# Performance work log

Hardware: AMD Instinct MI355X
Metric: run time of the kernel (lower is better)

## Reference

```python
import jax, jax.numpy as jnp
import numpy as np

C_ATOM = 128; C_PAIR = 16; H = 4; DH = 32; BQ = 32; BK = 128
N_ATOMS = 11776; NB = N_ATOMS // BQ; N_TOK = 512
C_TOK = 384; C_TP = 128; C_TP_IN = 32; N_LAYERS = 3

def _ln(x):
    mu = jnp.mean(x, axis=-1, keepdims=True)
    xc = x - mu
    var = jnp.mean(xc * xc, axis=-1, keepdims=True)
    return xc * jax.lax.rsqrt(var + 1e-5)

def setup_inputs():
    key = jax.random.key(0)
    ks = jax.random.split(key, 32)
    rn = lambda k, s, sc=0.02: jax.random.normal(k, s, jnp.float32) * sc
    q_idx = jnp.arange(N_ATOMS, dtype=jnp.int32).reshape(NB, BQ)
    centers = jnp.arange(NB, dtype=jnp.int32) * BQ + BQ // 2
    win = centers[:, None] + jnp.arange(-BK // 2, BK // 2, dtype=jnp.int32)[None, :]
    k_mask = (win >= 0) & (win < N_ATOMS)
    k_idx = jnp.clip(win, 0, N_ATOMS - 1)
    return {
        'atom_feats': jax.random.normal(ks[0], (1, N_ATOMS, C_ATOM), jnp.float32),
        'token_pair_feats': jax.random.normal(ks[1], (1, N_TOK, N_TOK, C_TP_IN), jnp.float32),
        'W_cond': rn(ks[2], (C_ATOM, C_ATOM)),
        'W_ph': rn(ks[3], (C_PAIR, C_ATOM)),
        'W_pw': rn(ks[4], (C_PAIR, C_ATOM)),
        'W_mlp1': rn(ks[5], (C_PAIR, C_PAIR)),
        'W_mlp2': rn(ks[6], (C_PAIR, C_PAIR)),
        'pb_ln_w': jnp.ones((C_PAIR,), jnp.float32),
        'pb_ln_b': jnp.zeros((C_PAIR,), jnp.float32),
        'pb_w': rn(ks[7], (H, C_PAIR)),
        'sln_w': rn(ks[8], (N_LAYERS, 2 * C_ATOM, C_ATOM)),
        'qkv_w': rn(ks[9], (N_LAYERS, 3 * C_ATOM, C_ATOM)),
        'q_bias': rn(ks[10], (N_LAYERS, C_ATOM)),
        'out_w': rn(ks[11], (N_LAYERS, C_ATOM, C_ATOM)),
        'out_b': jnp.zeros((N_LAYERS, C_ATOM), jnp.float32),
        'ada_w': rn(ks[12], (N_LAYERS, 2 * C_ATOM, C_ATOM)),
        'ta_w': rn(ks[13], (N_LAYERS, 4 * C_ATOM, C_ATOM)),
        'tb_w': rn(ks[14], (N_LAYERS, C_ATOM, 2 * C_ATOM)),
        'gate_w': rn(ks[15], (N_LAYERS, C_ATOM, C_ATOM)),
        'gate_b': jnp.full((N_LAYERS, C_ATOM), -2.0, jnp.float32),
        'W_tok': rn(ks[16], (C_TOK, C_ATOM)),
        'W_trunk': rn(ks[17], (C_TOK, C_TOK)),
        'W_struct': rn(ks[18], (C_TOK, C_TOK)),
        'W_pairin': rn(ks[19], (C_TP, C_TP_IN)),
        'W_outer': rn(ks[20], (2 * C_TP, C_TOK)),
        'q_idx': q_idx, 'k_idx': k_idx, 'k_mask': k_mask,
        'atom_to_token': jnp.sort(jax.random.randint(ks[21], (N_ATOMS,), 0, N_TOK, dtype=jnp.int32)),
    }

def _forward(atom_feats, token_pair_feats, W_cond, W_ph, W_pw, W_mlp1, W_mlp2,
             pb_ln_w, pb_ln_b, pb_w, sln_w, qkv_w, q_bias, out_w, out_b,
             ada_w, ta_w, tb_w, gate_w, gate_b, W_tok, W_trunk, W_struct,
             W_pairin, W_outer, q_idx, k_idx, k_mask, atom_to_token):
    c = atom_feats @ W_cond.T                       # [1,N,128] atom conditioning
    s_ln = _ln(c)                                   # shared normed conditioning
    # ---- blocked pair representation + pair-to-bias ----
    cq = jax.nn.relu(s_ln[:, q_idx])                # [1,NB,BQ,128]
    ck = jax.nn.relu(s_ln[:, k_idx])                # [1,NB,BK,128]
    p = (cq @ W_ph.T)[:, :, :, None, :] + (ck @ W_pw.T)[:, :, None, :, :]  # [1,NB,BQ,BK,16]
    p = p + jax.nn.relu(jax.nn.relu(p) @ W_mlp1.T) @ W_mlp2.T
    pb = (_ln(p) * pb_ln_w + pb_ln_b) @ pb_w.T      # [1,NB,BQ,BK,H]
    pb = jnp.transpose(pb, (0, 1, 4, 2, 3))         # [1,NB,H,BQ,BK]
    neg = jnp.where(k_mask[None, :, None, None, :], 0.0, -1e9)
    a = c
    scale = 1.0 / np.sqrt(DH).astype(np.float32)
    for l in range(N_LAYERS):
        # blocked local attention with AdaLN-conditioned input
        gb = s_ln @ sln_w[l].T
        x = jax.nn.sigmoid(gb[..., :C_ATOM]) * _ln(a) + gb[..., C_ATOM:]
        qkv = x @ qkv_w[l].T
        q, k, v = jnp.split(qkv, 3, axis=-1)
        q = (q + q_bias[l]).reshape(1, N_ATOMS, H, DH)
        k = k.reshape(1, N_ATOMS, H, DH)
        v = v.reshape(1, N_ATOMS, H, DH)
        qb = q[:, q_idx]; kb = k[:, k_idx]; vb = v[:, k_idx]
        sc = jnp.einsum('bnqhd,bnkhd->bnhqk', qb, kb) * scale + pb + neg
        att = jax.nn.softmax(sc, axis=-1)
        o = jnp.einsum('bnhqk,bnkhd->bnqhd', att, vb).reshape(1, N_ATOMS, C_ATOM)
        a = a + o @ out_w[l].T + out_b[l]
        # AdaLN-modulated SwiGLU transition with adaLN-zero gate (bias init -2)
        gb2 = s_ln @ ada_w[l].T
        xt = jax.nn.sigmoid(gb2[..., :C_ATOM]) * _ln(a) + gb2[..., C_ATOM:]
        ab = xt @ ta_w[l].T
        g = jax.nn.silu(ab[..., :2 * C_ATOM]) * ab[..., 2 * C_ATOM:]
        h = g @ tb_w[l].T
        gate = jax.nn.sigmoid(s_ln @ gate_w[l].T + gate_b[l])
        a = a + gate * h
    # ---- atom -> token aggregation and output projections ----
    atom_out = jax.nn.relu(a @ W_tok.T)             # [1,N,384]
    sums = jax.ops.segment_sum(atom_out[0], atom_to_token, num_segments=N_TOK)
    cnt = jax.ops.segment_sum(jnp.ones((N_ATOMS,), atom_out.dtype), atom_to_token, num_segments=N_TOK)
    tok = (sums / jnp.maximum(cnt, 1.0)[:, None])[None]  # [1,T,384]
    s_trunk = tok @ W_trunk.T
    s_struct = tok @ W_struct.T
    u = tok @ W_outer.T                              # [1,T,256]
    pair = token_pair_feats @ W_pairin.T + u[..., :C_TP][:, :, None, :] + u[..., C_TP:][:, None, :, :]
    return s_trunk, s_struct, pair

def reference(atom_feats, token_pair_feats, W_cond, W_ph, W_pw, W_mlp1, W_mlp2,
              pb_ln_w, pb_ln_b, pb_w, sln_w, qkv_w, q_bias, out_w, out_b,
              ada_w, ta_w, tb_w, gate_w, gate_b, W_tok, W_trunk, W_struct,
              W_pairin, W_outer, q_idx, k_idx, k_mask, atom_to_token):
    return _forward(atom_feats, token_pair_feats, W_cond, W_ph, W_pw, W_mlp1, W_mlp2,
                    pb_ln_w, pb_ln_b, pb_w, sln_w, qkv_w, q_bias, out_w, out_b,
                    ada_w, ta_w, tb_w, gate_w, gate_b, W_tok, W_trunk, W_struct,
                    W_pairin, W_outer, q_idx, k_idx, k_mask, atom_to_token)
```

## Files before the change

### kernel.cpp

```cpp
#include <hip/hip_runtime.h>
#include <cstddef>

typedef unsigned short u16;
typedef __attribute__((ext_vector_type(8))) short bf8;
typedef __attribute__((ext_vector_type(4))) float f4;
typedef __attribute__((ext_vector_type(4))) unsigned short us4;

#define NATOMS 11776
#define NBLK   368

__device__ __forceinline__ u16 f2b(float x){
  union { float f; unsigned u; } v; v.f = x;
  unsigned r = v.u + 0x7fffu + ((v.u >> 16) & 1u);
  return (u16)(r >> 16);
}
__device__ __forceinline__ float b2f(u16 x){
  union { unsigned u; float f; } v; v.u = ((unsigned)x) << 16;
  return v.f;
}
__device__ __forceinline__ f4 f4zero(){ f4 z = {0.f,0.f,0.f,0.f}; return z; }
__device__ __forceinline__ f4 mfma16(bf8 a, bf8 b, f4 c){
  return __builtin_amdgcn_mfma_f32_16x16x32_bf16(a, b, c, 0, 0, 0);
}
__device__ __forceinline__ int iclamp(int v, int lo, int hi){ return v < lo ? lo : (v > hi ? hi : v); }
__device__ __forceinline__ void lds_fence(){
  asm volatile("s_waitcnt lgkmcnt(0)" ::: "memory");
  __builtin_amdgcn_sched_barrier(0);
}
__device__ __forceinline__ bf8 cvt_f32x8(const float* __restrict__ p){
  float4 a = *(const float4*)p, b = *(const float4*)(p + 4);
  bf8 o;
  o[0] = (short)f2b(a.x); o[1] = (short)f2b(a.y); o[2] = (short)f2b(a.z); o[3] = (short)f2b(a.w);
  o[4] = (short)f2b(b.x); o[5] = (short)f2b(b.y); o[6] = (short)f2b(b.z); o[7] = (short)f2b(b.w);
  return o;
}

struct CvtArgs {
  const float* src[11];
  u16* dst[11];
  int n4[11];
};

__global__ __launch_bounds__(256) void k_convert(CvtArgs a){
  int stride = gridDim.x * 256;
  int tid = blockIdx.x * 256 + threadIdx.x;
  for (int s = 0; s < 11; ++s){
    const float4* src = (const float4*)a.src[s];
    us4* dst = (us4*)a.dst[s];
    int n = a.n4[s];
    for (int i = tid; i < n; i += stride){
      float4 v = src[i];
      us4 o;
      o.x = f2b(v.x); o.y = f2b(v.y); o.z = f2b(v.z); o.w = f2b(v.w);
      dst[i] = o;
    }
  }
}

template<int N, int K, int LDA = K>
__device__ __forceinline__ void gemm_strip(const u16* __restrict__ A, const u16* __restrict__ W, float* L){
  constexpr int CPW = N / 4;
  constexpr int T = CPW / 16;
  const int lane = threadIdx.x & 63;
  const int wave = threadIdx.x >> 6;
  const int rr = lane & 15, grp = lane >> 4;
  f4 acc[T];
#pragma unroll
  for (int t = 0; t < T; ++t) acc[t] = f4zero();
#pragma unroll
  for (int kc = 0; kc < K / 32; ++kc){
    bf8 af = *(const bf8*)(A + rr * LDA + kc * 32 + grp * 8);
#pragma unroll
    for (int t = 0; t < T; ++t){
      const u16* wp = W + (size_t)(wave * CPW + t * 16 + rr) * K + kc * 32 + grp * 8;
      acc[t] = mfma16(af, *(const bf8*)wp, acc[t]);
    }
  }
#pragma unroll
  for (int t = 0; t < T; ++t)
#pragma unroll
    for (int r = 0; r < 4; ++r)
      L[(grp * 4 + r) * N + wave * CPW + t * 16 + rr] = acc[t][r];
}

__global__ __launch_bounds__(256) void k_cond(const float* __restrict__ af, const float* __restrict__ Wc,
                                              const float* __restrict__ Wph, const float* __restrict__ Wpw,
                                              float* __restrict__ a_f, float* __restrict__ lnA,
                                              u16* __restrict__ sln_bf, float* __restrict__ ph,
                                              float* __restrict__ pw){
  __shared__ float LB[16 * 128];
  __shared__ __align__(16) u16 X[16 * 136];
  const int strip = blockIdx.x;
  const int lane = threadIdx.x & 63, wave = threadIdx.x >> 6;
  const int rr = lane & 15, grp = lane >> 4;
  {
    f4 acc[2];
    acc[0] = f4zero(); acc[1] = f4zero();
#pragma unroll
    for (int kc = 0; kc < 4; ++kc){
      bf8 afr = cvt_f32x8(af + (size_t)(strip * 16 + rr) * 128 + kc * 32 + grp * 8);
#pragma unroll
      for (int t = 0; t < 2; ++t){
        bf8 bfr = cvt_f32x8(Wc + (size_t)(wave * 32 + t * 16 + rr) * 128 + kc * 32 + grp * 8);
        acc[t] = mfma16(afr, bfr, acc[t]);
      }
    }
#pragma unroll
    for (int t = 0; t < 2; ++t)
#pragma unroll
      for (int r = 0; r < 4; ++r)
        LB[(grp * 4 + r) * 128 + wave * 32 + t * 16 + rr] = acc[t][r];
  }
  __syncthreads();
  {
    int r = threadIdx.x >> 4, s = threadIdx.x & 15;
    float sum = 0.f, sq = 0.f;
#pragma unroll
    for (int j = 0; j < 8; ++j){ float v = LB[r * 128 + s * 8 + j]; sum += v; sq += v * v; }
#pragma unroll
    for (int m = 1; m < 16; m <<= 1){ sum += __shfl_xor(sum, m); sq += __shfl_xor(sq, m); }
    float mu = sum * (1.f / 128.f);
    float var = sq * (1.f / 128.f) - mu * mu;
    float rs = rsqrtf(var + 1e-5f);
#pragma unroll
    for (int j = 0; j < 8; ++j){
      int c = s * 8 + j;
      float v = LB[r * 128 + c];
      size_t idx = (size_t)(strip * 16 + r) * 128 + c;
      a_f[idx] = v;
      float ln = (v - mu) * rs;
      lnA[idx] = ln;
      sln_bf[idx] = f2b(ln);
      X[r * 136 + c] = f2b(fmaxf(ln, 0.f));
    }
  }
  __syncthreads();
  if (wave < 2){
    const float* Wsel = wave ? Wpw : Wph;
    f4 acc = f4zero();
#pragma unroll
    for (int kc = 0; kc < 4; ++kc){
      bf8 afr = *(const bf8*)(&X[rr * 136 + kc * 32 + grp * 8]);
      bf8 bfr = cvt_f32x8(Wsel + (size_t)rr * 128 + kc * 32 + grp * 8);
      acc = mfma16(afr, bfr, acc);
    }
    float* out = wave ? pw : ph;
#pragma unroll
    for (int r = 0; r < 4; ++r)
      out[(size_t)(strip * 16 + grp * 4 + r) * 16 + rr] = acc[r];
  }
}

__global__ __launch_bounds__(256) void k_pre(const u16* __restrict__ sln, const float* __restrict__ lnA,
                                             const u16* __restrict__ slnW, const u16* __restrict__ qkvW,
                                             const float* __restrict__ qb, u16* __restrict__ qkv_out){
  __shared__ float LB[16 * 384];
  __shared__ __align__(16) u16 X[16 * 136];
  const int strip = blockIdx.x;
  const u16* Ag = sln + (size_t)strip * 2048;
  gemm_strip<256, 128>(Ag, slnW, LB);
  __syncthreads();
  for (int i = threadIdx.x; i < 2048; i += 256){
    int r = i >> 7, c = i & 127;
    float g1 = LB[r * 256 + c], g2 = LB[r * 256 + 128 + c];
    float s = 1.f / (1.f + __expf(-g1));
    X[r * 136 + c] = f2b(s * lnA[(size_t)(strip * 16 + r) * 128 + c] + g2);
  }
  __syncthreads();
  gemm_strip<384, 128, 136>(X, qkvW, LB);
  __syncthreads();
  const float scale = 0.17677669529663687f;
  for (int i = threadIdx.x; i < 16 * 384; i += 256){
    int r = i / 384, c = i - r * 384;
    float v = LB[i];
    if (c < 128) v = (v + qb[c]) * scale;
    qkv_out[(size_t)(strip * 16 + r) * 384 + c] = f2b(v);
  }
}

template<int LAST>
__global__ __launch_bounds__(256) void k_post(const u16* __restrict__ sln, float* __restrict__ lnA,
                                              float* __restrict__ a,
                                              const u16* __restrict__ gateW, const float* __restrict__ gbias,
                                              const u16* __restrict__ adaW, const u16* __restrict__ taW,
                                              const u16* __restrict__ tbW, const u16* __restrict__ tokW,
                                              float* __restrict__ atom_out){
  __shared__ float LB[16 * 512];
  __shared__ __align__(16) u16 X[16 * 136];
  __shared__ __align__(16) u16 G[16 * 264];
  const int strip = blockIdx.x;
  const u16* Ag = sln + (size_t)strip * 2048;
  float gv[8];
  gemm_strip<128, 128>(Ag, gateW, LB);
  __syncthreads();
#pragma unroll
  for (int ii = 0; ii < 8; ++ii){
    int i = threadIdx.x + 256 * ii;
    int c = i & 127;
    gv[ii] = 1.f / (1.f + __expf(-(LB[i] + gbias[c])));
  }
  __syncthreads();
  gemm_strip<256, 128>(Ag, adaW, LB);
  __syncthreads();
  for (int i = threadIdx.x; i < 2048; i += 256){
    int r = i >> 7, c = i & 127;
    float g1 = LB[r * 256 + c], g2 = LB[r * 256 + 128 + c];
    float s = 1.f / (1.f + __expf(-g1));
    X[r * 136 + c] = f2b(s * lnA[(size_t)(strip * 16 + r) * 128 + c] + g2);
  }
  __syncthreads();
  gemm_strip<512, 128, 136>(X, taW, LB);
  __syncthreads();
  for (int i = threadIdx.x; i < 16 * 256; i += 256){
    int r = i >> 8, c = i & 255;
    float ab1 = LB[r * 512 + c], ab2 = LB[r * 512 + 256 + c];
    G[r * 264 + c] = f2b(ab1 / (1.f + __expf(-ab1)) * ab2);
  }
  __syncthreads();
  gemm_strip<128, 256, 264>(G, tbW, LB);
  __syncthreads();
#pragma unroll
  for (int ii = 0; ii < 8; ++ii){
    int i = threadIdx.x + 256 * ii;
    size_t idx = (size_t)strip * 2048 + i;
    float v = a[idx] + gv[ii] * LB[i];
    a[idx] = v;
    LB[i] = v;
    if (LAST){ int r = i >> 7, c = i & 127; X[r * 136 + c] = f2b(v); }
  }
  __syncthreads();
  if (!LAST){
    int r = threadIdx.x >> 4, s = threadIdx.x & 15;
    float sum = 0.f, sq = 0.f;
#pragma unroll
    for (int j = 0; j < 8; ++j){ float v = LB[r * 128 + s * 8 + j]; sum += v; sq += v * v; }
#pragma unroll
    for (int m = 1; m < 16; m <<= 1){ sum += __shfl_xor(sum, m); sq += __shfl_xor(sq, m); }
    float mu = sum * (1.f / 128.f);
    float var = sq * (1.f / 128.f) - mu * mu;
    float rs = rsqrtf(var + 1e-5f);
#pragma unroll
    for (int j = 0; j < 8; ++j){
      int c = s * 8 + j;
      lnA[(size_t)(strip * 16 + r) * 128 + c] = (LB[r * 128 + c] - mu) * rs;
    }
  } else {
    gemm_strip<384, 128, 136>(X, tokW, LB);
    __syncthreads();
    const size_t base = (size_t)strip * 16 * 384;
    for (int i = threadIdx.x; i < 16 * 384; i += 256) atom_out[base + i] = fmaxf(LB[i], 0.f);
  }
}

__global__ __launch_bounds__(256) void k_pb(const float* __restrict__ ph, const float* __restrict__ pw,
                                            const float* __restrict__ W1, const float* __restrict__ W2,
                                            const float* __restrict__ lnw, const float* __restrict__ lnb,
                                            const float* __restrict__ pbw, float* __restrict__ bias){
  __shared__ __align__(16) u16 mt[4][16 * 24];
  __shared__ __align__(16) u16 vt[4][16 * 24];
  const int t = threadIdx.x;
  const int lane = t & 63, wave = t >> 6;
  const int rr = lane & 15, grp = lane >> 4;
  const int b = blockIdx.x >> 3, qg = blockIdx.x & 7;
  const int q = qg * 4 + wave;
  const int qa = b * 32 + q;

  bf8 wf1 = {0,0,0,0,0,0,0,0}, wf2 = {0,0,0,0,0,0,0,0};
  bf8 bproj = {0,0,0,0,0,0,0,0}, bones = {0,0,0,0,0,0,0,0};
  if (grp < 2){
#pragma unroll
    for (int j = 0; j < 8; ++j){
      wf1[j] = (short)f2b(W1[rr * 16 + grp * 8 + j]);
      wf2[j] = (short)f2b(W2[rr * 16 + grp * 8 + j]);
      bones[j] = (short)0x3F80;
    }
    if (rr < 4){
#pragma unroll
      for (int j = 0; j < 8; ++j)
        bproj[j] = (short)f2b(pbw[rr * 16 + grp * 8 + j] * lnw[grp * 8 + j]);
    }
  }
  float w2s_r = 0.f, bb_r = 0.f;
  if (rr < 4){
#pragma unroll
    for (int cc = 0; cc < 16; ++cc){
      float pv = pbw[rr * 16 + cc];
      w2s_r += pv * lnw[cc];
      bb_r  += pv * lnb[cc];
    }
  }
  const float* phq = ph + (size_t)qa * 16;
  float pha[8];
  if (grp < 2){
#pragma unroll
    for (int j = 0; j < 8; ++j) pha[j] = phq[grp * 8 + j];
  }
  const float ph_r = phq[rr];
  u16* mw = &mt[wave][0];
  u16* vw = &vt[wave][0];

  for (int kt = 0; kt < 8; ++kt){
    const int k0 = kt * 16;
    bf8 af = {0,0,0,0,0,0,0,0};
    if (grp < 2){
      int winA = b * 32 + k0 + rr - 48;
      int kaA = iclamp(winA, 0, NATOMS - 1);
      const float* pwr = pw + (size_t)kaA * 16 + grp * 8;
#pragma unroll
      for (int j = 0; j < 8; ++j) af[j] = (short)f2b(fmaxf(pha[j] + pwr[j], 0.f));
    }
    f4 c1 = mfma16(af, wf1, f4zero());
#pragma unroll
    for (int r = 0; r < 4; ++r)
      mw[(grp * 4 + r) * 24 + rr] = f2b(fmaxf(c1[r], 0.f));
    lds_fence();
    bf8 mf = {0,0,0,0,0,0,0,0};
    if (grp < 2) mf = *(const bf8*)(mw + rr * 24 + grp * 8);
    f4 c2 = mfma16(mf, wf2, f4zero());
#pragma unroll
    for (int r = 0; r < 4; ++r){
      int win = b * 32 + k0 + grp * 4 + r - 48;
      int ka = iclamp(win, 0, NATOMS - 1);
      float v = c2[r] + ph_r + pw[(size_t)ka * 16 + rr];
      vw[(grp * 4 + r) * 24 + rr] = f2b(v);
    }
    lds_fence();
    bf8 vf = {0,0,0,0,0,0,0,0}, vf2 = {0,0,0,0,0,0,0,0};
    if (grp < 2){
      vf = *(const bf8*)(vw + rr * 24 + grp * 8);
#pragma unroll
      for (int j = 0; j < 8; ++j){
        float x = b2f((u16)vf[j]);
        union { float f; unsigned u; } s; s.f = x * x;
        vf2[j] = (short)(u16)(s.u >> 16);
      }
    }
    f4 T1 = mfma16(vf, bproj, f4zero());
    f4 T2 = mfma16(vf, bones, f4zero());
    f4 T3 = mfma16(vf2, bones, f4zero());
    if (rr < 4){
      float4 o;
      float ov[4];
#pragma unroll
      for (int r = 0; r < 4; ++r){
        int win = b * 32 + k0 + grp * 4 + r - 48;
        bool valid = (win >= 0) && (win < NATOMS);
        float S = T2[r], Q = T3[r], d = T1[r];
        float mu = S * (1.f / 16.f);
        float var = Q * (1.f / 16.f) - mu * mu;
        float rq = rsqrtf(var + 1e-5f);
        ov[r] = rq * (d - mu * w2s_r) + bb_r + (valid ? 0.f : -1e9f);
      }
      o.x = ov[0]; o.y = ov[1]; o.z = ov[2]; o.w = ov[3];
      *(float4*)(bias + ((size_t)((b * 4 + rr) * 32) + q) * 128 + k0 + grp * 4) = o;
    }
  }
}

__global__ __launch_bounds__(256) void k_attn(const u16* __restrict__ qkv, const float* __restrict__ bias,
                                              const u16* __restrict__ outw, const float* __restrict__ outb,
                                              float* __restrict__ a, float* __restrict__ lnA){
  __shared__ u16 VT[128][136];
  __shared__ u16 P[4][32 * 136];
  __shared__ u16 O[32][136];
  __shared__ float part2[32][8];
  const int t = threadIdx.x;
  const int lane = t & 63, wave = t >> 6;
  const int b = blockIdx.x;
  const int rr = lane & 15, grp = lane >> 4;

  for (int i = 0; i < 8; ++i){
    int s = t + 256 * i;
    int ka = s & 127, d0 = (s >> 7) * 8;
    int win = b * 32 + ka - 48;
    int src = iclamp(win, 0, NATOMS - 1);
    bf8 v = *(const bf8*)(qkv + (size_t)src * 384 + 256 + d0);
#pragma unroll
    for (int j = 0; j < 8; ++j) VT[d0 + j][ka] = (u16)v[j];
  }
  __syncthreads();

  const int h = wave;
  bf8 kfr[8];
#pragma unroll
  for (int kt = 0; kt < 8; ++kt){
    int ka = kt * 16 + rr;
    int win = b * 32 + ka - 48;
    int src = iclamp(win, 0, NATOMS - 1);
    kfr[kt] = *(const bf8*)(qkv + (size_t)src * 384 + 128 + h * 32 + grp * 8);
  }
  f4 S[2][8];
#pragma unroll
  for (int qt = 0; qt < 2; ++qt){
    bf8 qf = *(const bf8*)(qkv + (size_t)(b * 32 + qt * 16 + rr) * 384 + h * 32 + grp * 8);
#pragma unroll
    for (int kt = 0; kt < 8; ++kt){
      S[qt][kt] = f4zero();
      S[qt][kt] = mfma16(qf, kfr[kt], S[qt][kt]);
    }
  }
  const float* brow = bias + (size_t)((b * 4 + h) * 32) * 128;
#pragma unroll
  for (int qt = 0; qt < 2; ++qt){
#pragma unroll
    for (int r = 0; r < 4; ++r){
      int q = qt * 16 + grp * 4 + r;
      float vals[8];
      float mx = -1e30f;
#pragma unroll
      for (int kt = 0; kt < 8; ++kt){
        float v = S[qt][kt][r] + brow[q * 128 + kt * 16 + rr];
        vals[kt] = v;
        mx = fmaxf(mx, v);
      }
#pragma unroll
      for (int m = 1; m < 16; m <<= 1) mx = fmaxf(mx, __shfl_xor(mx, m));
      float sum = 0.f;
#pragma unroll
      for (int kt = 0; kt < 8; ++kt){ vals[kt] = __expf(vals[kt] - mx); sum += vals[kt]; }
#pragma unroll
      for (int m = 1; m < 16; m <<= 1) sum += __shfl_xor(sum, m);
      float inv = 1.f / sum;
#pragma unroll
      for (int kt = 0; kt < 8; ++kt)
        P[h][q * 136 + kt * 16 + rr] = f2b(vals[kt] * inv);
    }
  }
  __syncthreads();
  f4 oacc[2][2];
#pragma unroll
  for (int qt = 0; qt < 2; ++qt)
#pragma unroll
    for (int dt = 0; dt < 2; ++dt) oacc[qt][dt] = f4zero();
#pragma unroll
  for (int kc = 0; kc < 4; ++kc){
#pragma unroll
    for (int qt = 0; qt < 2; ++qt){
      bf8 pa = *(const bf8*)(&P[h][(qt * 16 + rr) * 136 + kc * 32 + grp * 8]);
#pragma unroll
      for (int dt = 0; dt < 2; ++dt){
        bf8 vb = *(const bf8*)(&VT[h * 32 + dt * 16 + rr][kc * 32 + grp * 8]);
        oacc[qt][dt] = mfma16(pa, vb, oacc[qt][dt]);
      }
    }
  }
#pragma unroll
  for (int qt = 0; qt < 2; ++qt)
#pragma unroll
    for (int dt = 0; dt < 2; ++dt)
#pragma unroll
      for (int r = 0; r < 4; ++r)
        O[qt * 16 + grp * 4 + r][h * 32 + dt * 16 + rr] = f2b(oacc[qt][dt][r]);
  __syncthreads();
  f4 pacc[2][2];
#pragma unroll
  for (int qt = 0; qt < 2; ++qt)
#pragma unroll
    for (int ct = 0; ct < 2; ++ct) pacc[qt][ct] = f4zero();
#pragma unroll
  for (int kc = 0; kc < 4; ++kc){
    bf8 a0 = *(const bf8*)(&O[rr][kc * 32 + grp * 8]);
    bf8 a1 = *(const bf8*)(&O[16 + rr][kc * 32 + grp * 8]);
#pragma unroll
    for (int ct = 0; ct < 2; ++ct){
      bf8 wf = *(const bf8*)(outw + (size_t)(wave * 32 + ct * 16 + rr) * 128 + kc * 32 + grp * 8);
      pacc[0][ct] = mfma16(a0, wf, pacc[0][ct]);
      pacc[1][ct] = mfma16(a1, wf, pacc[1][ct]);
    }
  }
  float vv[2][2][4];
#pragma unroll
  for (int qt = 0; qt < 2; ++qt)
#pragma unroll
    for (int ct = 0; ct < 2; ++ct)
#pragma unroll
      for (int r = 0; r < 4; ++r){
        int q = qt * 16 + grp * 4 + r;
        int col = wave * 32 + ct * 16 + rr;
        size_t idx = (size_t)(b * 32 + q) * 128 + col;
        float v = a[idx] + pacc[qt][ct][r] + outb[col];
        a[idx] = v;
        vv[qt][ct][r] = v;
      }
#pragma unroll
  for (int qt = 0; qt < 2; ++qt)
#pragma unroll
    for (int r = 0; r < 4; ++r){
      float ps = vv[qt][0][r] + vv[qt][1][r];
      float pq = vv[qt][0][r] * vv[qt][0][r] + vv[qt][1][r] * vv[qt][1][r];
#pragma unroll
      for (int m = 1; m < 16; m <<= 1){ ps += __shfl_xor(ps, m); pq += __shfl_xor(pq, m); }
      if (rr == 0){
        int q = qt * 16 + grp * 4 + r;
        part2[q][wave * 2] = ps;
        part2[q][wave * 2 + 1] = pq;
      }
    }
  __syncthreads();
#pragma unroll
  for (int qt = 0; qt < 2; ++qt)
#pragma unroll
    for (int r = 0; r < 4; ++r){
      int q = qt * 16 + grp * 4 + r;
      f4 p0 = *(const f4*)&part2[q][0];
      f4 p1 = *(const f4*)&part2[q][4];
      float S = p0[0] + p0[2] + p1[0] + p1[2];
      float Q = p0[1] + p0[3] + p1[1] + p1[3];
      float mu = S * (1.f / 128.f);
      float var = Q * (1.f / 128.f) - mu * mu;
      float rs = rsqrtf(var + 1e-5f);
#pragma unroll
      for (int ct = 0; ct < 2; ++ct){
        int col = wave * 32 + ct * 16 + rr;
        lnA[(size_t)(b * 32 + q) * 128 + col] = (vv[qt][ct][r] - mu) * rs;
      }
    }
}

__device__ __forceinline__ int lbound(const int* __restrict__ arr, int n, int v){
  int lo = 0, hi = n;
  while (lo < hi){ int mid = (lo + hi) >> 1; if (arr[mid] < v) lo = mid + 1; else hi = mid; }
  return lo;
}

__global__ __launch_bounds__(256) void k_segmean(const float* __restrict__ atom_out,
                                                 const int* __restrict__ a2t, u16* __restrict__ tokbf){
  const int tok = blockIdx.x;
  __shared__ int lo_s, hi_s;
  if (threadIdx.x == 0){
    lo_s = lbound(a2t, NATOMS, tok);
    hi_s = lbound(a2t, NATOMS, tok + 1);
  }
  __syncthreads();
  int lo = lo_s, hi = hi_s;
  float inv = 1.f / fmaxf((float)(hi - lo), 1.f);
  for (int c = threadIdx.x; c < 384; c += 256){
    float s = 0.f;
    for (int aa = lo; aa < hi; ++aa) s += atom_out[(size_t)aa * 384 + c];
    tokbf[(size_t)tok * 384 + c] = f2b(s * inv);
  }
}

__global__ __launch_bounds__(256) void k_tok(const u16* __restrict__ tok, const u16* __restrict__ catW,
                                             float* __restrict__ s_trunk, float* __restrict__ s_struct,
                                             float* __restrict__ u_f){
  __shared__ float LB[16 * 1024];
  const int strip = blockIdx.x;
  gemm_strip<1024, 384>(tok + (size_t)strip * 16 * 384, catW, LB);
  __syncthreads();
  for (int i = threadIdx.x; i < 16 * 1024; i += 256){
    int r = i >> 10, c = i & 1023;
    int row = strip * 16 + r;
    float v = LB[i];
    if (c < 384) s_trunk[(size_t)row * 384 + c] = v;
    else if (c < 768) s_struct[(size_t)row * 384 + (c - 384)] = v;
    else u_f[(size_t)row * 256 + (c - 768)] = v;
  }
}

__global__ __launch_bounds__(256) void k_pair(const float* __restrict__ tpf, const float* __restrict__ Wp,
                                              const float* __restrict__ u, float* __restrict__ out){
  const int lane = threadIdx.x & 63, wave = threadIdx.x >> 6;
  const int rr = lane & 15, grp = lane >> 4;
  const int pairbase = blockIdx.x * 64 + wave * 16;
  const int i = (blockIdx.x * 64) >> 9;
  bf8 af;
  {
    const float* tr = tpf + (size_t)(pairbase + rr) * 32 + grp * 8;
#pragma unroll
    for (int j = 0; j < 8; ++j) af[j] = (short)f2b(tr[j]);
  }
  f4 acc[8];
#pragma unroll
  for (int t = 0; t < 8; ++t){
    bf8 bf;
    const float* wr = Wp + (size_t)(t * 16 + rr) * 32 + grp * 8;
#pragma unroll
    for (int j = 0; j < 8; ++j) bf[j] = (short)f2b(wr[j]);
    acc[t] = mfma16(af, bf, f4zero());
  }
  const float* ui = u + (size_t)i * 256;
#pragma unroll
  for (int t = 0; t < 8; ++t){
    int c = t * 16 + rr;
    float uic = ui[c];
#pragma unroll
    for (int r = 0; r < 4; ++r){
      int p = pairbase + grp * 4 + r;
      int j = p & 511;
      out[(size_t)p * 128 + c] = acc[t][r] + uic + u[(size_t)j * 256 + 128 + c];
    }
  }
}

extern "C" void kernel_launch(void* const* d_in, const int* in_sizes, int n_in,
                              void* d_out, int out_size, void* d_ws, size_t ws_size,
                              hipStream_t stream){
  (void)in_sizes; (void)n_in; (void)out_size; (void)ws_size;
  const float* atom_feats = (const float*)d_in[0];
  const float* tpf        = (const float*)d_in[1];
  const float* W_cond     = (const float*)d_in[2];
  const float* W_ph       = (const float*)d_in[3];
  const float* W_pw       = (const float*)d_in[4];
  const float* W_mlp1     = (const float*)d_in[5];
  const float* W_mlp2     = (const float*)d_in[6];
  const float* pb_ln_w    = (const float*)d_in[7];
  const float* pb_ln_b    = (const float*)d_in[8];
  const float* pb_w       = (const float*)d_in[9];
  const float* sln_w      = (const float*)d_in[10];
  const float* qkv_w      = (const float*)d_in[11];
  const float* q_bias     = (const float*)d_in[12];
  const float* out_w      = (const float*)d_in[13];
  const float* out_b      = (const float*)d_in[14];
  const float* ada_w      = (const float*)d_in[15];
  const float* ta_w       = (const float*)d_in[16];
  const float* tb_w       = (const float*)d_in[17];
  const float* gate_w     = (const float*)d_in[18];
  const float* gate_b     = (const float*)d_in[19];
  const float* W_tok      = (const float*)d_in[20];
  const float* W_trunk    = (const float*)d_in[21];
  const float* W_struct   = (const float*)d_in[22];
  const float* W_pairin   = (const float*)d_in[23];
  const float* W_outer    = (const float*)d_in[24];
  const int*   a2t        = (const int*)d_in[28];

  char* wsb = (char*)d_ws;
  size_t off = 0;
  auto alc = [&](size_t bytes) -> void* {
    void* r = wsb + off;
    off = (off + bytes + 255) & ~(size_t)255;
    return r;
  };

  u16* sln_bfw   = (u16*)alc(98304 * 2);
  u16* qkv_bfw   = (u16*)alc(147456 * 2);
  u16* out_bfw   = (u16*)alc(49152 * 2);
  u16* ada_bfw   = (u16*)alc(98304 * 2);
  u16* ta_bfw    = (u16*)alc(196608 * 2);
  u16* tb_bfw    = (u16*)alc(98304 * 2);
  u16* gate_bfw  = (u16*)alc(49152 * 2);
  u16* tok_bfw   = (u16*)alc(49152 * 2);
  u16* trunk_bfw = (u16*)alc(147456 * 2);
  u16* struct_bfw= (u16*)alc(147456 * 2);
  u16* outer_bfw = (u16*)alc(98304 * 2);
  float* a_f     = (float*)alc((size_t)NATOMS * 128 * 4);
  float* lnA     = (float*)alc((size_t)NATOMS * 128 * 4);
  u16* sln_bf    = (u16*)alc((size_t)NATOMS * 128 * 2);
  u16* qkv_bf    = (u16*)alc((size_t)NATOMS * 384 * 2);
  float* ph      = (float*)alc((size_t)NATOMS * 16 * 4);
  float* pw      = (float*)alc((size_t)NATOMS * 16 * 4);
  float* bias    = (float*)alc((size_t)NBLK * 4 * 32 * 128 * 4);
  float* atom_out= bias;
  u16* tok_bf    = (u16*)alc(512 * 384 * 2);
  float* u_f     = (float*)alc(512 * 256 * 4);

  float* s_trunk  = (float*)d_out;
  float* s_struct = s_trunk + 512 * 384;
  float* pair_out = s_struct + 512 * 384;

  CvtArgs ca;
  const float* srcs[11] = {sln_w, qkv_w, out_w, ada_w, ta_w, tb_w, gate_w,
                           W_tok, W_trunk, W_struct, W_outer};
  u16* dsts[11] = {sln_bfw, qkv_bfw, out_bfw, ada_bfw, ta_bfw, tb_bfw, gate_bfw,
                   tok_bfw, trunk_bfw, struct_bfw, outer_bfw};
  int n4s[11] = {24576, 36864, 12288, 24576, 49152, 24576, 12288,
                 12288, 36864, 36864, 24576};
  for (int s = 0; s < 11; ++s){ ca.src[s] = srcs[s]; ca.dst[s] = dsts[s]; ca.n4[s] = n4s[s]; }
  k_convert<<<256, 256, 0, stream>>>(ca);

  k_cond<<<736, 256, 0, stream>>>(atom_feats, W_cond, W_ph, W_pw, a_f, lnA, sln_bf, ph, pw);
  k_pb<<<NBLK * 8, 256, 0, stream>>>(ph, pw, W_mlp1, W_mlp2, pb_ln_w, pb_ln_b, pb_w, bias);

  for (int l = 0; l < 3; ++l){
    const u16* slnW  = sln_bfw  + (size_t)l * 256 * 128;
    const u16* qkvW  = qkv_bfw  + (size_t)l * 384 * 128;
    const u16* outW  = out_bfw  + (size_t)l * 128 * 128;
    const u16* adaW  = ada_bfw  + (size_t)l * 256 * 128;
    const u16* taW   = ta_bfw   + (size_t)l * 512 * 128;
    const u16* tbW   = tb_bfw   + (size_t)l * 128 * 256;
    const u16* gateW = gate_bfw + (size_t)l * 128 * 128;
    k_pre<<<736, 256, 0, stream>>>(sln_bf, lnA, slnW, qkvW, q_bias + l * 128, qkv_bf);
    k_attn<<<NBLK, 256, 0, stream>>>(qkv_bf, bias, outW, out_b + l * 128, a_f, lnA);
    if (l < 2)
      k_post<0><<<736, 256, 0, stream>>>(sln_bf, lnA, a_f, gateW, gate_b + l * 128,
                                         adaW, taW, tbW, tok_bfw, atom_out);
    else
      k_post<1><<<736, 256, 0, stream>>>(sln_bf, lnA, a_f, gateW, gate_b + l * 128,
                                         adaW, taW, tbW, tok_bfw, atom_out);
  }

  k_segmean<<<512, 256, 0, stream>>>(atom_out, a2t, tok_bf);
  k_tok<<<32, 256, 0, stream>>>(tok_bf, trunk_bfw, s_trunk, s_struct, u_f);
  k_pair<<<4096, 256, 0, stream>>>(tpf, W_pairin, u_f, pair_out);
}
```

Before: 390.6 us.

## Fuse per-layer pre-attention projection into cond and post kernels; split token GEMM

The pre-attention kernel (adaptive LN gating plus QKV projection) is folded into the tail of the conditioning kernel for layer 0 and into the post-attention kernel for later layers. The normalized activations stay in shared memory instead of being written to lnA and read back, and three kernel launches are removed. Separately, the token projection kernel is split across four column quadrants, giving 128 blocks instead of 32 for more parallelism. The fused kernels use more shared memory per block, which may lower occupancy.

```diff
diff --git a/kernel.cpp b/kernel.cpp
--- a/kernel.cpp
+++ b/kernel.cpp
@@ -83,13 +83,17 @@
       L[(grp * 4 + r) * N + wave * CPW + t * 16 + rr] = acc[t][r];
 }
 
-__global__ __launch_bounds__(256) void k_cond(const float* __restrict__ af, const float* __restrict__ Wc,
-                                              const float* __restrict__ Wph, const float* __restrict__ Wpw,
-                                              float* __restrict__ a_f, float* __restrict__ lnA,
-                                              u16* __restrict__ sln_bf, float* __restrict__ ph,
-                                              float* __restrict__ pw){
-  __shared__ float LB[16 * 128];
-  __shared__ __align__(16) u16 X[16 * 136];
+__global__ __launch_bounds__(256) void k_cond_pre(const float* __restrict__ af, const float* __restrict__ Wc,
+                                                  const float* __restrict__ Wph, const float* __restrict__ Wpw,
+                                                  float* __restrict__ a_f, u16* __restrict__ sln_bf,
+                                                  float* __restrict__ ph, float* __restrict__ pw,
+                                                  const u16* __restrict__ slnW, const u16* __restrict__ qkvW,
+                                                  const float* __restrict__ qb, u16* __restrict__ qkv_out){
+  __shared__ float LB[16 * 384];
+  __shared__ __align__(16) u16 Xs[16 * 136];
+  __shared__ __align__(16) u16 Xr[16 * 136];
+  __shared__ __align__(16) u16 Xx[16 * 136];
+  __shared__ float LNf[16 * 128];
   const int strip = blockIdx.x;
   const int lane = threadIdx.x & 63, wave = threadIdx.x >> 6;
   const int rr = lane & 15, grp = lane >> 4;
@@ -129,45 +133,24 @@
       size_t idx = (size_t)(strip * 16 + r) * 128 + c;
       a_f[idx] = v;
       float ln = (v - mu) * rs;
-      lnA[idx] = ln;
-      sln_bf[idx] = f2b(ln);
-      X[r * 136 + c] = f2b(fmaxf(ln, 0.f));
-    }
-  }
-  __syncthreads();
-  if (wave < 2){
-    const float* Wsel = wave ? Wpw : Wph;
-    f4 acc = f4zero();
-#pragma unroll
-    for (int kc = 0; kc < 4; ++kc){
-      bf8 afr = *(const bf8*)(&X[rr * 136 + kc * 32 + grp * 8]);
-      bf8 bfr = cvt_f32x8(Wsel + (size_t)rr * 128 + kc * 32 + grp * 8);
-      acc = mfma16(afr, bfr, acc);
-    }
-    float* out = wave ? pw : ph;
-#pragma unroll
-    for (int r = 0; r < 4; ++r)
-      out[(size_t)(strip * 16 + grp * 4 + r) * 16 + rr] = acc[r];
-  }
-}
-
-__global__ __launch_bounds__(256) void k_pre(const u16* __restrict__ sln, const float* __restrict__ lnA,
-                                             const u16* __restrict__ slnW, const u16* __restrict__ qkvW,
-                                             const float* __restrict__ qb, u16* __restrict__ qkv_out){
-  __shared__ float LB[16 * 384];
-  __shared__ __align__(16) u16 X[16 * 136];
-  const int strip = blockIdx.x;
-  const u16* Ag = sln + (size_t)strip * 2048;
-  gemm_strip<256, 128>(Ag, slnW, LB);
+      LNf[r * 128 + c] = ln;
+      u16 lb = f2b(ln);
+      sln_bf[idx] = lb;
+      Xs[r * 136 + c] = lb;
+      Xr[r * 136 + c] = f2b(fmaxf(ln, 0.f));
+    }
+  }
+  __syncthreads();
+  gemm_strip<256, 128, 136>(Xs, slnW, LB);
   __syncthreads();
   for (int i = threadIdx.x; i < 2048; i += 256){
     int r = i >> 7, c = i & 127;
     float g1 = LB[r * 256 + c], g2 = LB[r * 256 + 128 + c];
     float s = 1.f / (1.f + __expf(-g1));
-    X[r * 136 + c] = f2b(s * lnA[(size_t)(strip * 16 + r) * 128 + c] + g2);
-  }
-  __syncthreads();
-  gemm_strip<384, 128, 136>(X, qkvW, LB);
+    Xx[r * 136 + c] = f2b(s * LNf[r * 128 + c] + g2);
+  }
+  __syncthreads();
+  gemm_strip<384, 128, 136>(Xx, qkvW, LB);
   __syncthreads();
   const float scale = 0.17677669529663687f;
   for (int i = threadIdx.x; i < 16 * 384; i += 256){
@@ -176,18 +159,35 @@
     if (c < 128) v = (v + qb[c]) * scale;
     qkv_out[(size_t)(strip * 16 + r) * 384 + c] = f2b(v);
   }
+  if (wave < 2){
+    const float* Wsel = wave ? Wpw : Wph;
+    f4 acc = f4zero();
+#pragma unroll
+    for (int kc = 0; kc < 4; ++kc){
+      bf8 afr = *(const bf8*)(&Xr[rr * 136 + kc * 32 + grp * 8]);
+      bf8 bfr = cvt_f32x8(Wsel + (size_t)rr * 128 + kc * 32 + grp * 8);
+      acc = mfma16(afr, bfr, acc);
+    }
+    float* out = wave ? pw : ph;
+#pragma unroll
+    for (int r = 0; r < 4; ++r)
+      out[(size_t)(strip * 16 + grp * 4 + r) * 16 + rr] = acc[r];
+  }
 }
 
 template<int LAST>
-__global__ __launch_bounds__(256) void k_post(const u16* __restrict__ sln, float* __restrict__ lnA,
-                                              float* __restrict__ a,
-                                              const u16* __restrict__ gateW, const float* __restrict__ gbias,
-                                              const u16* __restrict__ adaW, const u16* __restrict__ taW,
-                                              const u16* __restrict__ tbW, const u16* __restrict__ tokW,
-                                              float* __restrict__ atom_out){
+__global__ __launch_bounds__(256) void k_postpre(const u16* __restrict__ sln, const float* __restrict__ lnA,
+                                                 float* __restrict__ a,
+                                                 const u16* __restrict__ gateW, const float* __restrict__ gbias,
+                                                 const u16* __restrict__ adaW, const u16* __restrict__ taW,
+                                                 const u16* __restrict__ tbW,
+                                                 const u16* __restrict__ slnW2, const u16* __restrict__ qkvW2,
+                                                 const float* __restrict__ qb2, u16* __restrict__ qkv_out,
+                                                 const u16* __restrict__ tokW, float* __restrict__ atom_out){
   __shared__ float LB[16 * 512];
   __shared__ __align__(16) u16 X[16 * 136];
   __shared__ __align__(16) u16 G[16 * 264];
+  __shared__ float LNf[16 * 128];
   const int strip = blockIdx.x;
   const u16* Ag = sln + (size_t)strip * 2048;
   float gv[8];
@@ -230,19 +230,40 @@
   }
   __syncthreads();
   if (!LAST){
-    int r = threadIdx.x >> 4, s = threadIdx.x & 15;
-    float sum = 0.f, sq = 0.f;
-#pragma unroll
-    for (int j = 0; j < 8; ++j){ float v = LB[r * 128 + s * 8 + j]; sum += v; sq += v * v; }
-#pragma unroll
-    for (int m = 1; m < 16; m <<= 1){ sum += __shfl_xor(sum, m); sq += __shfl_xor(sq, m); }
-    float mu = sum * (1.f / 128.f);
-    float var = sq * (1.f / 128.f) - mu * mu;
-    float rs = rsqrtf(var + 1e-5f);
-#pragma unroll
-    for (int j = 0; j < 8; ++j){
-      int c = s * 8 + j;
-      lnA[(size_t)(strip * 16 + r) * 128 + c] = (LB[r * 128 + c] - mu) * rs;
+    {
+      int r = threadIdx.x >> 4, s = threadIdx.x & 15;
+      float sum = 0.f, sq = 0.f;
+#pragma unroll
+      for (int j = 0; j < 8; ++j){ float v = LB[r * 128 + s * 8 + j]; sum += v; sq += v * v; }
+#pragma unroll
+      for (int m = 1; m < 16; m <<= 1){ sum += __shfl_xor(sum, m); sq += __shfl_xor(sq, m); }
+      float mu = sum * (1.f / 128.f);
+      float var = sq * (1.f / 128.f) - mu * mu;
+      float rs = rsqrtf(var + 1e-5f);
+#pragma unroll
+      for (int j = 0; j < 8; ++j){
+        int c = s * 8 + j;
+        LNf[r * 128 + c] = (LB[r * 128 + c] - mu) * rs;
+      }
+    }
+    __syncthreads();
+    gemm_strip<256, 128>(Ag, slnW2, LB);
+    __syncthreads();
+    for (int i = threadIdx.x; i < 2048; i += 256){
+      int r = i >> 7, c = i & 127;
+      float g1 = LB[r * 256 + c], g2 = LB[r * 256 + 128 + c];
+      float s = 1.f / (1.f + __expf(-g1));
+      X[r * 136 + c] = f2b(s * LNf[r * 128 + c] + g2);
+    }
+    __syncthreads();
+    gemm_strip<384, 128, 136>(X, qkvW2, LB);
+    __syncthreads();
+    const float scale = 0.17677669529663687f;
+    for (int i = threadIdx.x; i < 16 * 384; i += 256){
+      int r = i / 384, c = i - r * 384;
+      float v = LB[i];
+      if (c < 128) v = (v + qb2[c]) * scale;
+      qkv_out[(size_t)(strip * 16 + r) * 384 + c] = f2b(v);
     }
   } else {
     gemm_strip<384, 128, 136>(X, tokW, LB);
@@ -544,17 +565,18 @@
 __global__ __launch_bounds__(256) void k_tok(const u16* __restrict__ tok, const u16* __restrict__ catW,
                                              float* __restrict__ s_trunk, float* __restrict__ s_struct,
                                              float* __restrict__ u_f){
-  __shared__ float LB[16 * 1024];
-  const int strip = blockIdx.x;
-  gemm_strip<1024, 384>(tok + (size_t)strip * 16 * 384, catW, LB);
-  __syncthreads();
-  for (int i = threadIdx.x; i < 16 * 1024; i += 256){
-    int r = i >> 10, c = i & 1023;
+  __shared__ float LB[16 * 256];
+  const int strip = blockIdx.x >> 2, quad = blockIdx.x & 3;
+  gemm_strip<256, 384>(tok + (size_t)strip * 16 * 384, catW + (size_t)quad * 256 * 384, LB);
+  __syncthreads();
+  for (int i = threadIdx.x; i < 16 * 256; i += 256){
+    int r = i >> 8, c = i & 255;
     int row = strip * 16 + r;
+    int cg = quad * 256 + c;
     float v = LB[i];
-    if (c < 384) s_trunk[(size_t)row * 384 + c] = v;
-    else if (c < 768) s_struct[(size_t)row * 384 + (c - 384)] = v;
-    else u_f[(size_t)row * 256 + (c - 768)] = v;
+    if (cg < 384) s_trunk[(size_t)row * 384 + cg] = v;
+    else if (cg < 768) s_struct[(size_t)row * 384 + (cg - 384)] = v;
+    else u_f[(size_t)row * 256 + (cg - 768)] = v;
   }
 }
 
@@ -668,28 +690,33 @@
   for (int s = 0; s < 11; ++s){ ca.src[s] = srcs[s]; ca.dst[s] = dsts[s]; ca.n4[s] = n4s[s]; }
   k_convert<<<256, 256, 0, stream>>>(ca);
 
-  k_cond<<<736, 256, 0, stream>>>(atom_feats, W_cond, W_ph, W_pw, a_f, lnA, sln_bf, ph, pw);
+  k_cond_pre<<<736, 256, 0, stream>>>(atom_feats, W_cond, W_ph, W_pw, a_f, sln_bf, ph, pw,
+                                      sln_bfw, qkv_bfw, q_bias, qkv_bf);
   k_pb<<<NBLK * 8, 256, 0, stream>>>(ph, pw, W_mlp1, W_mlp2, pb_ln_w, pb_ln_b, pb_w, bias);
 
   for (int l = 0; l < 3; ++l){
-    const u16* slnW  = sln_bfw  + (size_t)l * 256 * 128;
-    const u16* qkvW  = qkv_bfw  + (size_t)l * 384 * 128;
     const u16* outW  = out_bfw  + (size_t)l * 128 * 128;
     const u16* adaW  = ada_bfw  + (size_t)l * 256 * 128;
     const u16* taW   = ta_bfw   + (size_t)l * 512 * 128;
     const u16* tbW   = tb_bfw   + (size_t)l * 128 * 256;
     const u16* gateW = gate_bfw + (size_t)l * 128 * 128;
-    k_pre<<<736, 256, 0, stream>>>(sln_bf, lnA, slnW, qkvW, q_bias + l * 128, qkv_bf);
     k_attn<<<NBLK, 256, 0, stream>>>(qkv_bf, bias, outW, out_b + l * 128, a_f, lnA);
-    if (l < 2)
-      k_post<0><<<736, 256, 0, stream>>>(sln_bf, lnA, a_f, gateW, gate_b + l * 128,
-                                         adaW, taW, tbW, tok_bfw, atom_out);
-    else
-      k_post<1><<<736, 256, 0, stream>>>(sln_bf, lnA, a_f, gateW, gate_b + l * 128,
-                                         adaW, taW, tbW, tok_bfw, atom_out);
+    if (l < 2){
+      const u16* slnW2 = sln_bfw + (size_t)(l + 1) * 256 * 128;
+      const u16* qkvW2 = qkv_bfw + (size_t)(l + 1) * 384 * 128;
+      k_postpre<0><<<736, 256, 0, stream>>>(sln_bf, lnA, a_f, gateW, gate_b + l * 128,
+                                            adaW, taW, tbW, slnW2, qkvW2,
+                                            q_bias + (l + 1) * 128, qkv_bf,
+                                            nullptr, nullptr);
+    } else {
+      k_postpre<1><<<736, 256, 0, stream>>>(sln_bf, lnA, a_f, gateW, gate_b + l * 128,
+                                            adaW, taW, tbW, nullptr, nullptr,
+                                            nullptr, nullptr,
+                                            tok_bfw, atom_out);
+    }
   }
 
   k_segmean<<<512, 256, 0, stream>>>(atom_out, a2t, tok_bf);
-  k_tok<<<32, 256, 0, stream>>>(tok_bf, trunk_bfw, s_trunk, s_struct, u_f);
+  k_tok<<<128, 256, 0, stream>>>(tok_bf, trunk_bfw, s_trunk, s_struct, u_f);
   k_pair<<<4096, 256, 0, stream>>>(tpf, W_pairin, u_f, pair_out);
 }
```

After: 354.1 us. -9.3%, faster.
